# Kernel optimization log

Measured on AMD Instinct MI355X. Metric: run time of the kernel, lower is better.

The kernel has to match this reference:

```python
import jax, jax.numpy as jnp
import numpy as np

N_NODES = 50000
N_EDGES = 400000
NFEAT, NHID, NOUT, NCLASS = 512, 256, 256, 8


def _glorot(key, shape):
    lim = float(np.sqrt(6.0 / (shape[0] + shape[1])))
    return jax.random.uniform(key, shape, jnp.float32, -lim, lim)


def setup_inputs() -> dict:
    key = jax.random.key(0)
    ks = jax.random.split(key, 8)
    x = jax.random.normal(ks[0], (N_NODES, NFEAT), jnp.float32)
    edge_index = jax.random.randint(ks[1], (2, N_EDGES), 0, N_NODES, jnp.int32)
    # learnable edge weight logits (init 1 - eps in the module; trained => generic values)
    edge_w_params = jnp.ones((N_EDGES,), jnp.float32) * 0.9999
    W1 = _glorot(ks[2], (NFEAT, NHID)); b1 = jnp.zeros((NHID,), jnp.float32)
    W2 = _glorot(ks[3], (NHID, NHID)); b2 = jnp.zeros((NHID,), jnp.float32)
    W3 = _glorot(ks[4], (NHID, NOUT)); b3 = jnp.zeros((NOUT,), jnp.float32)
    Wlin = _glorot(ks[5], (NHID + NHID + NOUT, NCLASS))
    blin = jnp.zeros((NCLASS,), jnp.float32)
    return {"x": x, "edge_index": edge_index, "edge_w_params": edge_w_params,
            "W1": W1, "b1": b1, "W2": W2, "b2": b2, "W3": W3, "b3": b3,
            "Wlin": Wlin, "blin": blin}


def _gcn_conv(x, W, b, src, dst, ew, n):
    """PyG GCNConv with add_self_loops=True.
    Self-loop weight is 1 (fill_value). norm = d^-1/2[src] * w * d^-1/2[dst].
    Self-loop contribution handled analytically (no edge concat).
    """
    deg = jax.ops.segment_sum(ew, dst, num_segments=n) + 1.0  # +1 self-loop weight
    dinv = jnp.where(deg > 0, jax.lax.rsqrt(deg), 0.0)
    norm = dinv[src] * ew * dinv[dst]                          # [E]
    h = x @ W                                                  # [n, out]
    agg = jax.ops.segment_sum(h[src] * norm[:, None], dst, num_segments=n)
    agg = agg + h * (dinv * dinv)[:, None]                     # self loops
    return agg + b


def reference(x, edge_index, edge_w_params, W1, b1, W2, b2, W3, b3, Wlin, blin):
    n = x.shape[0]
    src, dst = edge_index[0], edge_index[1]
    ew = jax.nn.sigmoid(edge_w_params)
    ones_ew = jnp.ones_like(ew)
    x1 = jax.nn.relu(_gcn_conv(x, W1, b1, src, dst, ew, n))    # dropout: eval mode (identity)
    x2 = jax.nn.relu(_gcn_conv(x1, W2, b2, src, dst, ew, n))
    x3 = _gcn_conv(x2, W3, b3, src, dst, ones_ew, n)           # gc3 called without edge_weight
    logits = jnp.concatenate((x1, x2, x3), axis=1) @ Wlin + blin
    return jax.nn.log_softmax(logits, axis=1)
```

## Files before the change

kernel.cpp:

```cpp
#include <hip/hip_runtime.h>
#include <math.h>

#define N_NODES 50000
#define N_EDGES 400000
#define M_PAD 50048
#define NFEAT 512
#define NHID 256
#define NCLASS 8
#define SCAN_BLOCKS ((N_NODES + 255) / 256)

typedef unsigned short u16;
typedef __attribute__((ext_vector_type(8))) unsigned short u16x8;
typedef __attribute__((ext_vector_type(8))) short s16x8;
typedef __attribute__((ext_vector_type(4))) float f32x4;

__device__ __forceinline__ float bf2f(u16 u) {
    union { unsigned int i; float f; } v; v.i = ((unsigned int)u) << 16; return v.f;
}
__device__ __forceinline__ float bf2f_hi(unsigned int packed) {
    union { unsigned int i; float f; } v; v.i = packed & 0xffff0000u; return v.f;
}
__device__ __forceinline__ float bf2f_lo(unsigned int packed) {
    union { unsigned int i; float f; } v; v.i = packed << 16; return v.f;
}
__device__ __forceinline__ u16 f2bf(float f) {
    union { float f; unsigned int i; } v; v.f = f;
    unsigned int r = v.i + 0x7fffu + ((v.i >> 16) & 1u);
    return (u16)(r >> 16);
}


__global__ void init_k(float* deg, int* cnt, int* cur) {
    int i = blockIdx.x * blockDim.x + threadIdx.x;
    if (i < N_NODES) { deg[i] = 1.0f; cnt[i] = 0; cur[i] = 0; }
}

__global__ void edge_deg_k(const float* __restrict__ p, const int* __restrict__ dst,
                           float* __restrict__ deg, int* __restrict__ cnt,
                           float* __restrict__ ew_out) {
    int e = blockIdx.x * blockDim.x + threadIdx.x;
    if (e >= N_EDGES) return;
    float ew = 1.0f / (1.0f + expf(-p[e]));
    ew_out[e] = ew;
    int d = dst[e];
    atomicAdd(&deg[d], ew);
    atomicAdd(&cnt[d], 1);
}

__global__ void finalize_dinv_k(float* __restrict__ deg, const int* __restrict__ cnt,
                                float* __restrict__ dinv3) {
    int i = blockIdx.x * blockDim.x + threadIdx.x;
    if (i < N_NODES) {
        deg[i]   = 1.0f / sqrtf(deg[i]);
        dinv3[i] = 1.0f / sqrtf(1.0f + (float)cnt[i]);
    }
}

__global__ __launch_bounds__(256) void scan1_k(const int* __restrict__ cnt,
                                               int* __restrict__ row_start,
                                               int* __restrict__ bsum) {
    __shared__ int tmp[256];
    int t = threadIdx.x;
    int g = blockIdx.x * 256 + t;
    int v = (g < N_NODES) ? cnt[g] : 0;
    tmp[t] = v;
    __syncthreads();
    #pragma unroll
    for (int off = 1; off < 256; off <<= 1) {
        int u = (t >= off) ? tmp[t - off] : 0;
        __syncthreads();
        tmp[t] += u;
        __syncthreads();
    }
    if (g < N_NODES) row_start[g] = tmp[t] - v;
    if (t == 255) bsum[blockIdx.x] = tmp[255];
}

__global__ __launch_bounds__(256) void scan2_k(int* __restrict__ bsum,
                                               int* __restrict__ row_start) {
    __shared__ int tmp[256];
    int t = threadIdx.x;
    int v = (t < SCAN_BLOCKS) ? bsum[t] : 0;
    tmp[t] = v;
    __syncthreads();
    #pragma unroll
    for (int off = 1; off < 256; off <<= 1) {
        int u = (t >= off) ? tmp[t - off] : 0;
        __syncthreads();
        tmp[t] += u;
        __syncthreads();
    }
    if (t < SCAN_BLOCKS) bsum[t] = tmp[t] - v;
    if (t == SCAN_BLOCKS - 1) row_start[N_NODES] = v;
}

__global__ void fill_k(const int* __restrict__ src, const int* __restrict__ dst,
                       const float* __restrict__ ew, const float* __restrict__ dinv,
                       const float* __restrict__ dinv3,
                       const int* __restrict__ row_start, const int* __restrict__ bsum,
                       int* __restrict__ cur,
                       uint2* __restrict__ ep, uint2* __restrict__ ep3) {
    int e = blockIdx.x * blockDim.x + threadIdx.x;
    if (e >= N_EDGES) return;
    int s = src[e], d = dst[e];
    float w  = dinv[s] * ew[e] * dinv[d];
    float w3 = dinv3[s] * dinv3[d];
    int p = atomicAdd(&cur[d], 1);
    int slot = row_start[d] + bsum[d >> 8] + p;
    ep[slot]  = make_uint2((unsigned int)s, __float_as_uint(w));
    ep3[slot] = make_uint2((unsigned int)s, __float_as_uint(w3));
}


#define WT_TOTAL (256 * 512 + 2 * 256 * 256)
#define ZP_TOTAL ((M_PAD - N_NODES) * 256)

__global__ void wtrans_zp_k(const float* __restrict__ W1, const float* __restrict__ W2,
                            const float* __restrict__ W3, u16* __restrict__ wt1,
                            u16* __restrict__ wt2, u16* __restrict__ wt3,
                            u16* __restrict__ zp_a, u16* __restrict__ zp_b) {
    int idx = blockIdx.x * 256 + threadIdx.x;
    if (idx < WT_TOTAL) {
        const float* W; u16* Wt; int K;
        if (idx < 256 * 512)                  { W = W1; Wt = wt1; K = 512; }
        else if (idx < 256 * 512 + 256 * 256) { idx -= 256 * 512; W = W2; Wt = wt2; K = 256; }
        else                                  { idx -= 256 * 512 + 256 * 256; W = W3; Wt = wt3; K = 256; }
        int n = idx / K, k = idx - n * K;
        Wt[(size_t)n * K + k] = f2bf(W[(size_t)k * 256 + n]);
        return;
    }
    int z = idx - WT_TOTAL;
    if (z < ZP_TOTAL) {
        zp_a[(size_t)N_NODES * 256 + z] = 0;
        zp_b[(size_t)N_NODES * 256 + z] = 0;
    }
}


__device__ __forceinline__ u16x8 ldcvt_f32(const float* p, bool ok) {
    u16x8 o = {0, 0, 0, 0, 0, 0, 0, 0};
    if (ok) {
        float4 a = *(const float4*)p;
        float4 b = *(const float4*)(p + 4);
        o[0] = f2bf(a.x); o[1] = f2bf(a.y); o[2] = f2bf(a.z); o[3] = f2bf(a.w);
        o[4] = f2bf(b.x); o[5] = f2bf(b.y); o[6] = f2bf(b.z); o[7] = f2bf(b.w);
    }
    return o;
}

template <bool AF32>
__global__ __launch_bounds__(256) void gemm_bf16_k(const void* __restrict__ Ap,
                                                   const u16* __restrict__ BT,
                                                   u16* __restrict__ C, int K) {
    __shared__ u16 Asl[128 * 40];
    __shared__ u16 Bsl[128 * 40];
    int tid = threadIdx.x;
    int lane = tid & 63;
    int wid = tid >> 6;
    int wm = wid >> 1, wn = wid & 1;
    int row0 = blockIdx.x * 128;
    int col0 = blockIdx.y * 128;

    int c0 = tid, c1 = tid + 256;
    int ar0 = c0 >> 2, ak0 = (c0 & 3) << 3;
    int ar1 = c1 >> 2, ak1 = (c1 & 3) << 3;
    const u16*   A16 = (const u16*)Ap;
    const float* A32 = (const float*)Ap;
    bool ok0 = (row0 + ar0) < N_NODES;
    bool ok1 = (row0 + ar1) < N_NODES;
    const u16* Ag0 = A16 + (size_t)(row0 + ar0) * K + ak0;
    const u16* Ag1 = A16 + (size_t)(row0 + ar1) * K + ak1;
    const float* Af0 = A32 + (size_t)(row0 + ar0) * K + ak0;
    const float* Af1 = A32 + (size_t)(row0 + ar1) * K + ak1;
    const u16* Bg0 = BT + (size_t)(col0 + ar0) * K + ak0;
    const u16* Bg1 = BT + (size_t)(col0 + ar1) * K + ak1;
    int la0 = ar0 * 40 + ak0, la1 = ar1 * 40 + ak1;

    u16x8 ra0, ra1, rb0, rb1;
    if (AF32) { ra0 = ldcvt_f32(Af0, ok0); ra1 = ldcvt_f32(Af1, ok1); }
    else      { ra0 = *(const u16x8*)Ag0;  ra1 = *(const u16x8*)Ag1; }
    rb0 = *(const u16x8*)Bg0;
    rb1 = *(const u16x8*)Bg1;

    f32x4 acc[4][4] = {};
    int arow = wm * 64 + (lane & 15);
    int bcol = wn * 64 + (lane & 15);
    int kg = (lane >> 4) << 3;

    int nt = K >> 5;
    for (int t = 0; t < nt; ++t) {
        __syncthreads();
        *(u16x8*)&Asl[la0] = ra0; *(u16x8*)&Asl[la1] = ra1;
        *(u16x8*)&Bsl[la0] = rb0; *(u16x8*)&Bsl[la1] = rb1;
        __syncthreads();
        if (t + 1 < nt) {
            int ko = (t + 1) << 5;
            if (AF32) { ra0 = ldcvt_f32(Af0 + ko, ok0); ra1 = ldcvt_f32(Af1 + ko, ok1); }
            else      { ra0 = *(const u16x8*)(Ag0 + ko); ra1 = *(const u16x8*)(Ag1 + ko); }
            rb0 = *(const u16x8*)(Bg0 + ko);
            rb1 = *(const u16x8*)(Bg1 + ko);
        }
        s16x8 af[4], bf[4];
        #pragma unroll
        for (int m = 0; m < 4; ++m)
            af[m] = *(const s16x8*)&Asl[(arow + m * 16) * 40 + kg];
        #pragma unroll
        for (int n = 0; n < 4; ++n)
            bf[n] = *(const s16x8*)&Bsl[(bcol + n * 16) * 40 + kg];
        #pragma unroll
        for (int m = 0; m < 4; ++m)
            #pragma unroll
            for (int n = 0; n < 4; ++n)
                acc[m][n] = __builtin_amdgcn_mfma_f32_16x16x32_bf16(af[m], bf[n], acc[m][n], 0, 0, 0);
    }

    int crow0 = row0 + wm * 64 + ((lane >> 4) << 2);
    int ccol  = col0 + wn * 64 + (lane & 15);
    #pragma unroll
    for (int m = 0; m < 4; ++m)
        #pragma unroll
        for (int n = 0; n < 4; ++n)
            #pragma unroll
            for (int r = 0; r < 4; ++r)
                C[(size_t)(crow0 + m * 16 + r) * 256 + ccol + n * 16] = f2bf(acc[m][n][r]);
}


__device__ __forceinline__ void fma4(float4& acc, uint2 u, float w) {
    acc.x += bf2f_lo(u.x) * w; acc.y += bf2f_hi(u.x) * w;
    acc.z += bf2f_lo(u.y) * w; acc.w += bf2f_hi(u.y) * w;
}

template <bool RELU>
__global__ __launch_bounds__(256) void gather_k(const u16* __restrict__ h,
                                                const int* __restrict__ row_start,
                                                const int* __restrict__ bsum,
                                                const uint2* __restrict__ ep,
                                                const float* __restrict__ dinv,
                                                const float* __restrict__ bias,
                                                u16* __restrict__ outb) {
    int node = blockIdx.x * 4 + (threadIdx.x >> 6);
    if (node >= N_NODES) return;
    int lane = threadIdx.x & 63;

    float di = dinv[node];
    float sw = di * di;
    uint2 hv = *(const uint2*)(h + (size_t)node * 256 + lane * 4);
    float4 acc;
    acc.x = bf2f_lo(hv.x) * sw; acc.y = bf2f_hi(hv.x) * sw;
    acc.z = bf2f_lo(hv.y) * sw; acc.w = bf2f_hi(hv.y) * sw;

    int beg = row_start[node] + bsum[node >> 8];
    int end = row_start[node + 1] + bsum[(node + 1) >> 8];
    int j = beg;
    for (; j + 8 <= end; j += 8) {
        uint2 e0 = ep[j],     e1 = ep[j + 1], e2 = ep[j + 2], e3 = ep[j + 3];
        uint2 e4 = ep[j + 4], e5 = ep[j + 5], e6 = ep[j + 6], e7 = ep[j + 7];
        uint2 u0 = *(const uint2*)(h + (size_t)e0.x * 256 + lane * 4);
        uint2 u1 = *(const uint2*)(h + (size_t)e1.x * 256 + lane * 4);
        uint2 u2 = *(const uint2*)(h + (size_t)e2.x * 256 + lane * 4);
        uint2 u3 = *(const uint2*)(h + (size_t)e3.x * 256 + lane * 4);
        uint2 u4 = *(const uint2*)(h + (size_t)e4.x * 256 + lane * 4);
        uint2 u5 = *(const uint2*)(h + (size_t)e5.x * 256 + lane * 4);
        uint2 u6 = *(const uint2*)(h + (size_t)e6.x * 256 + lane * 4);
        uint2 u7 = *(const uint2*)(h + (size_t)e7.x * 256 + lane * 4);
        fma4(acc, u0, __uint_as_float(e0.y)); fma4(acc, u1, __uint_as_float(e1.y));
        fma4(acc, u2, __uint_as_float(e2.y)); fma4(acc, u3, __uint_as_float(e3.y));
        fma4(acc, u4, __uint_as_float(e4.y)); fma4(acc, u5, __uint_as_float(e5.y));
        fma4(acc, u6, __uint_as_float(e6.y)); fma4(acc, u7, __uint_as_float(e7.y));
    }
    for (; j + 4 <= end; j += 4) {
        uint2 e0 = ep[j], e1 = ep[j + 1], e2 = ep[j + 2], e3 = ep[j + 3];
        uint2 u0 = *(const uint2*)(h + (size_t)e0.x * 256 + lane * 4);
        uint2 u1 = *(const uint2*)(h + (size_t)e1.x * 256 + lane * 4);
        uint2 u2 = *(const uint2*)(h + (size_t)e2.x * 256 + lane * 4);
        uint2 u3 = *(const uint2*)(h + (size_t)e3.x * 256 + lane * 4);
        fma4(acc, u0, __uint_as_float(e0.y)); fma4(acc, u1, __uint_as_float(e1.y));
        fma4(acc, u2, __uint_as_float(e2.y)); fma4(acc, u3, __uint_as_float(e3.y));
    }
    for (; j < end; ++j) {
        uint2 e = ep[j];
        uint2 u = *(const uint2*)(h + (size_t)e.x * 256 + lane * 4);
        fma4(acc, u, __uint_as_float(e.y));
    }
    float4 bv = ((const float4*)bias)[lane];
    acc.x += bv.x; acc.y += bv.y; acc.z += bv.z; acc.w += bv.w;
    if (RELU) {
        acc.x = fmaxf(acc.x, 0.f); acc.y = fmaxf(acc.y, 0.f);
        acc.z = fmaxf(acc.z, 0.f); acc.w = fmaxf(acc.w, 0.f);
    }
    uint2 o;
    o.x = (unsigned int)f2bf(acc.x) | ((unsigned int)f2bf(acc.y) << 16);
    o.y = (unsigned int)f2bf(acc.z) | ((unsigned int)f2bf(acc.w) << 16);
    *(uint2*)(outb + (size_t)node * 256 + lane * 4) = o;
}


template <int MODE>
__global__ __launch_bounds__(256) void logits_acc_k(const u16* __restrict__ x,
                                                    const float* __restrict__ Wlin,
                                                    const float* __restrict__ blin,
                                                    float* __restrict__ logits,
                                                    float* __restrict__ out, int seg) {
    __shared__ float Ws[256 * 8];
    int tid = threadIdx.x;
    const float* Wseg = Wlin + (size_t)seg * 256 * 8;
    for (int i = tid; i < 2048; i += 256) Ws[i] = Wseg[i];
    __syncthreads();
    int row = blockIdx.x * 32 + (tid >> 3);
    int c = tid & 7;
    if (row >= N_NODES) return;
    const u16* xr = x + (size_t)row * 256;
    float acc = 0.f;
    for (int k8 = 0; k8 < 32; ++k8) {
        u16x8 v = *(const u16x8*)&xr[k8 * 8];
        #pragma unroll
        for (int i = 0; i < 8; ++i) acc += bf2f(v[i]) * Ws[(k8 * 8 + i) * 8 + c];
    }
    float* lp = &logits[(size_t)row * 8 + c];
    if (MODE == 0) {
        *lp = acc + blin[c];
    } else if (MODE == 1) {
        *lp += acc;
    } else {
        float t = *lp + acc;
        float m = t;
        m = fmaxf(m, __shfl_xor(m, 1));
        m = fmaxf(m, __shfl_xor(m, 2));
        m = fmaxf(m, __shfl_xor(m, 4));
        float s = expf(t - m);
        s += __shfl_xor(s, 1);
        s += __shfl_xor(s, 2);
        s += __shfl_xor(s, 4);
        out[(size_t)row * 8 + c] = t - (logf(s) + m);
    }
}


extern "C" void kernel_launch(void* const* d_in, const int* in_sizes, int n_in,
                              void* d_out, int out_size, void* d_ws, size_t ws_size,
                              hipStream_t stream) {
    const float* x    = (const float*)d_in[0];
    const int*   ei   = (const int*)d_in[1];
    const float* ewp  = (const float*)d_in[2];
    const float* W1   = (const float*)d_in[3];
    const float* b1   = (const float*)d_in[4];
    const float* W2   = (const float*)d_in[5];
    const float* b2   = (const float*)d_in[6];
    const float* W3   = (const float*)d_in[7];
    const float* b3   = (const float*)d_in[8];
    const float* Wlin = (const float*)d_in[9];
    const float* blin = (const float*)d_in[10];
    float* out = (float*)d_out;

    const int* src = ei;
    const int* dst = ei + N_EDGES;

    float* ws = (float*)d_ws;
    float* ew     = ws;
    float* dinv   = ew + N_EDGES;
    float* dinv3  = dinv + N_NODES;
    float* logits = dinv3 + N_NODES;
    int* cnt       = (int*)(logits + (size_t)N_NODES * 8);
    int* cur       = cnt + N_NODES;
    int* row_start = cur + N_NODES;
    int* bsum      = row_start + N_NODES + 1;
    uint2* ep  = (uint2*)(((uintptr_t)(bsum + SCAN_BLOCKS) + 127) & ~(uintptr_t)127);
    uint2* ep3 = ep + N_EDGES;
    u16* hb  = (u16*)(ep3 + N_EDGES);
    u16* x1b = hb  + (size_t)M_PAD * 256;
    u16* x2b = x1b + (size_t)M_PAD * 256;
    u16* x3b = x2b + (size_t)M_PAD * 256;
    u16* wt1 = x3b + (size_t)M_PAD * 256;
    u16* wt2 = wt1 + 256 * 512;
    u16* wt3 = wt2 + 256 * 256;

    dim3 blk(256);
    int nodeBlocks  = (N_NODES + 255) / 256;
    int edgeBlocks  = (N_EDGES + 255) / 256;
    int gathBlocks  = (N_NODES + 3) / 4;
    int rowBlocks32 = (N_NODES + 31) / 32;
    dim3 gemmGrid(M_PAD / 128, 2);

    init_k<<<nodeBlocks, blk, 0, stream>>>(dinv, cnt, cur);
    edge_deg_k<<<edgeBlocks, blk, 0, stream>>>(ewp, dst, dinv, cnt, ew);
    finalize_dinv_k<<<nodeBlocks, blk, 0, stream>>>(dinv, cnt, dinv3);
    scan1_k<<<SCAN_BLOCKS, blk, 0, stream>>>(cnt, row_start, bsum);
    scan2_k<<<1, blk, 0, stream>>>(bsum, row_start);
    fill_k<<<edgeBlocks, blk, 0, stream>>>(src, dst, ew, dinv, dinv3, row_start, bsum,
                                           cur, ep, ep3);

    wtrans_zp_k<<<(WT_TOTAL + ZP_TOTAL + 255) / 256, blk, 0, stream>>>(
        W1, W2, W3, wt1, wt2, wt3, x1b, x2b);

    gemm_bf16_k<true><<<gemmGrid, blk, 0, stream>>>(x, wt1, hb, NFEAT);
    gather_k<true><<<gathBlocks, blk, 0, stream>>>(hb, row_start, bsum, ep, dinv, b1, x1b);
    logits_acc_k<0><<<rowBlocks32, blk, 0, stream>>>(x1b, Wlin, blin, logits, nullptr, 0);

    gemm_bf16_k<false><<<gemmGrid, blk, 0, stream>>>(x1b, wt2, hb, NHID);
    gather_k<true><<<gathBlocks, blk, 0, stream>>>(hb, row_start, bsum, ep, dinv, b2, x2b);
    logits_acc_k<1><<<rowBlocks32, blk, 0, stream>>>(x2b, Wlin, blin, logits, nullptr, 1);

    gemm_bf16_k<false><<<gemmGrid, blk, 0, stream>>>(x2b, wt3, hb, NHID);
    gather_k<false><<<gathBlocks, blk, 0, stream>>>(hb, row_start, bsum, ep3, dinv3, b3, x3b);
    logits_acc_k<2><<<rowBlocks32, blk, 0, stream>>>(x3b, Wlin, blin, logits, out, 2);
}
```

Measured before the change: 311.8 us.

## Rewrite GEMM to keep a full-K B panel resident in LDS, streaming A from registers

Replaces the 128x128 tiled GEMM, which staged both A and B through shared memory, with a persistent-style kernel. Each block loads a 64-column slice of the transposed weights for the whole K into XOR-swizzled LDS once, then loops over row panels. Each wave reads its A fragments directly from global memory into registers with a two-stage software pipeline, so the main loop has no __syncthreads. This removes the per-k-tile barriers and A staging, at the cost of large LDS use (64 KB for K=512), which limits occupancy, and of uncoalesced-looking direct A loads.

```diff
diff --git a/kernel.cpp b/kernel.cpp
--- a/kernel.cpp
+++ b/kernel.cpp
@@ -148,81 +148,83 @@
     return o;
 }
 
-template <bool AF32>
-__global__ __launch_bounds__(256) void gemm_bf16_k(const void* __restrict__ Ap,
-                                                   const u16* __restrict__ BT,
-                                                   u16* __restrict__ C, int K) {
-    __shared__ u16 Asl[128 * 40];
-    __shared__ u16 Bsl[128 * 40];
-    int tid = threadIdx.x;
-    int lane = tid & 63;
-    int wid = tid >> 6;
-    int wm = wid >> 1, wn = wid & 1;
-    int row0 = blockIdx.x * 128;
-    int col0 = blockIdx.y * 128;
-
-    int c0 = tid, c1 = tid + 256;
-    int ar0 = c0 >> 2, ak0 = (c0 & 3) << 3;
-    int ar1 = c1 >> 2, ak1 = (c1 & 3) << 3;
+#define LOADA(AV, T)                                                            \
+    do {                                                                        \
+        _Pragma("unroll")                                                       \
+        for (int m = 0; m < 2; ++m) {                                           \
+            if constexpr (AF32) AV[m] = (s16x8)ldcvt_f32(ap32[m] + (T) * 32, ok[m]); \
+            else                AV[m] = *(const s16x8*)(ap16[m] + (T) * 32);    \
+        }                                                                       \
+    } while (0)
+
+#define BSTEP(AV, T)                                                            \
+    do {                                                                        \
+        int ko = ((T) * 32 + kg) ^ sw;      \
+        s16x8 bf[4];                                                            \
+        _Pragma("unroll")                                                       \
+        for (int n = 0; n < 4; ++n)                                             \
+            bf[n] = *(const s16x8*)&Bsl[(n * 16 + fr) * K + ko];                \
+        _Pragma("unroll")                                                       \
+        for (int m = 0; m < 2; ++m)                                             \
+            _Pragma("unroll")                                                   \
+            for (int n = 0; n < 4; ++n)                                         \
+                acc[m][n] = __builtin_amdgcn_mfma_f32_16x16x32_bf16(AV[m], bf[n], acc[m][n], 0, 0, 0); \
+    } while (0)
+
+template <bool AF32, int K>
+__global__ __launch_bounds__(256) void gemm_bp_k(const void* __restrict__ Ap,
+                                                 const u16* __restrict__ BT,
+                                                 u16* __restrict__ C, int GY) {
+    __shared__ u16 Bsl[64 * K];
+    int tid = threadIdx.x, lane = tid & 63, wid = tid >> 6;
+    int colbase = blockIdx.x * 64;
+    const int kchunks = K >> 3;
+
+    for (int i = tid; i < 64 * kchunks; i += 256) {
+        int col = i / kchunks;
+        int kc = (i - col * kchunks) << 3;
+        *(u16x8*)&Bsl[col * K + (kc ^ ((col & 7) << 3))] =
+            *(const u16x8*)&BT[(size_t)(colbase + col) * K + kc];
+    }
+    __syncthreads();
+
+    int fr = lane & 15;
+    int kg = (lane >> 4) << 3;
+    int sw = (fr & 7) << 3;
     const u16*   A16 = (const u16*)Ap;
     const float* A32 = (const float*)Ap;
-    bool ok0 = (row0 + ar0) < N_NODES;
-    bool ok1 = (row0 + ar1) < N_NODES;
-    const u16* Ag0 = A16 + (size_t)(row0 + ar0) * K + ak0;
-    const u16* Ag1 = A16 + (size_t)(row0 + ar1) * K + ak1;
-    const float* Af0 = A32 + (size_t)(row0 + ar0) * K + ak0;
-    const float* Af1 = A32 + (size_t)(row0 + ar1) * K + ak1;
-    const u16* Bg0 = BT + (size_t)(col0 + ar0) * K + ak0;
-    const u16* Bg1 = BT + (size_t)(col0 + ar1) * K + ak1;
-    int la0 = ar0 * 40 + ak0, la1 = ar1 * 40 + ak1;
-
-    u16x8 ra0, ra1, rb0, rb1;
-    if (AF32) { ra0 = ldcvt_f32(Af0, ok0); ra1 = ldcvt_f32(Af1, ok1); }
-    else      { ra0 = *(const u16x8*)Ag0;  ra1 = *(const u16x8*)Ag1; }
-    rb0 = *(const u16x8*)Bg0;
-    rb1 = *(const u16x8*)Bg1;
-
-    f32x4 acc[4][4] = {};
-    int arow = wm * 64 + (lane & 15);
-    int bcol = wn * 64 + (lane & 15);
-    int kg = (lane >> 4) << 3;
-
-    int nt = K >> 5;
-    for (int t = 0; t < nt; ++t) {
-        __syncthreads();
-        *(u16x8*)&Asl[la0] = ra0; *(u16x8*)&Asl[la1] = ra1;
-        *(u16x8*)&Bsl[la0] = rb0; *(u16x8*)&Bsl[la1] = rb1;
-        __syncthreads();
-        if (t + 1 < nt) {
-            int ko = (t + 1) << 5;
-            if (AF32) { ra0 = ldcvt_f32(Af0 + ko, ok0); ra1 = ldcvt_f32(Af1 + ko, ok1); }
-            else      { ra0 = *(const u16x8*)(Ag0 + ko); ra1 = *(const u16x8*)(Ag1 + ko); }
-            rb0 = *(const u16x8*)(Bg0 + ko);
-            rb1 = *(const u16x8*)(Bg1 + ko);
+    const int nt = K >> 5;
+
+    for (int p = blockIdx.y; p < M_PAD / 128; p += GY) {
+        int row0 = p * 128 + wid * 32;
+        const u16* ap16[2]; const float* ap32[2]; bool ok[2];
+        #pragma unroll
+        for (int m = 0; m < 2; ++m) {
+            int gr = row0 + m * 16 + fr;
+            ok[m]   = gr < N_NODES;
+            ap16[m] = A16 + (size_t)gr * K + kg;
+            ap32[m] = A32 + (size_t)gr * K + kg;
         }
-        s16x8 af[4], bf[4];
+        f32x4 acc[2][4] = {};
+        s16x8 aa[2], ab[2];
+        LOADA(aa, 0);
         #pragma unroll
-        for (int m = 0; m < 4; ++m)
-            af[m] = *(const s16x8*)&Asl[(arow + m * 16) * 40 + kg];
+        for (int t = 0; t < nt; t += 2) {
+            LOADA(ab, t + 1);
+            BSTEP(aa, t);
+            if (t + 2 < nt) LOADA(aa, t + 2);
+            BSTEP(ab, t + 1);
+        }
+        int crow0 = row0 + ((lane >> 4) << 2);
+        int ccol  = colbase + fr;
         #pragma unroll
-        for (int n = 0; n < 4; ++n)
-            bf[n] = *(const s16x8*)&Bsl[(bcol + n * 16) * 40 + kg];
-        #pragma unroll
-        for (int m = 0; m < 4; ++m)
+        for (int m = 0; m < 2; ++m)
             #pragma unroll
             for (int n = 0; n < 4; ++n)
-                acc[m][n] = __builtin_amdgcn_mfma_f32_16x16x32_bf16(af[m], bf[n], acc[m][n], 0, 0, 0);
-    }
-
-    int crow0 = row0 + wm * 64 + ((lane >> 4) << 2);
-    int ccol  = col0 + wn * 64 + (lane & 15);
-    #pragma unroll
-    for (int m = 0; m < 4; ++m)
-        #pragma unroll
-        for (int n = 0; n < 4; ++n)
-            #pragma unroll
-            for (int r = 0; r < 4; ++r)
-                C[(size_t)(crow0 + m * 16 + r) * 256 + ccol + n * 16] = f2bf(acc[m][n][r]);
+                #pragma unroll
+                for (int r = 0; r < 4; ++r)
+                    C[(size_t)(crow0 + m * 16 + r) * 256 + ccol + n * 16] = f2bf(acc[m][n][r]);
+    }
 }
 
 
@@ -380,7 +382,6 @@
     int edgeBlocks  = (N_EDGES + 255) / 256;
     int gathBlocks  = (N_NODES + 3) / 4;
     int rowBlocks32 = (N_NODES + 31) / 32;
-    dim3 gemmGrid(M_PAD / 128, 2);
 
     init_k<<<nodeBlocks, blk, 0, stream>>>(dinv, cnt, cur);
     edge_deg_k<<<edgeBlocks, blk, 0, stream>>>(ewp, dst, dinv, cnt, ew);
@@ -393,15 +394,15 @@
     wtrans_zp_k<<<(WT_TOTAL + ZP_TOTAL + 255) / 256, blk, 0, stream>>>(
         W1, W2, W3, wt1, wt2, wt3, x1b, x2b);
 
-    gemm_bf16_k<true><<<gemmGrid, blk, 0, stream>>>(x, wt1, hb, NFEAT);
+    gemm_bp_k<true, 512><<<dim3(4, 128), blk, 0, stream>>>(x, wt1, hb, 128);
     gather_k<true><<<gathBlocks, blk, 0, stream>>>(hb, row_start, bsum, ep, dinv, b1, x1b);
     logits_acc_k<0><<<rowBlocks32, blk, 0, stream>>>(x1b, Wlin, blin, logits, nullptr, 0);
 
-    gemm_bf16_k<false><<<gemmGrid, blk, 0, stream>>>(x1b, wt2, hb, NHID);
+    gemm_bp_k<false, 256><<<dim3(4, 256), blk, 0, stream>>>(x1b, wt2, hb, 256);
     gather_k<true><<<gathBlocks, blk, 0, stream>>>(hb, row_start, bsum, ep, dinv, b2, x2b);
     logits_acc_k<1><<<rowBlocks32, blk, 0, stream>>>(x2b, Wlin, blin, logits, nullptr, 1);
 
-    gemm_bf16_k<false><<<gemmGrid, blk, 0, stream>>>(x2b, wt3, hb, NHID);
+    gemm_bp_k<false, 256><<<dim3(4, 256), blk, 0, stream>>>(x2b, wt3, hb, 256);
     gather_k<false><<<gathBlocks, blk, 0, stream>>>(hb, row_start, bsum, ep3, dinv3, b3, x3b);
     logits_acc_k<2><<<rowBlocks32, blk, 0, stream>>>(x3b, Wlin, blin, logits, out, 2);
 }
```

Result: slower. 388.1 us (+24.5%).
